# Optimization experiments

Hardware: AMD Instinct MI355X
Metric: run time of the kernel (lower is better)

Reference implementation:

```python
import jax, jax.numpy as jnp
import numpy as np

B = 32768
SEQ_LEN = 24
H = 64            # HIDDEN_DIM
SLOTS = 8         # MEMORY_SLOTS
VOCAB = 64        # VOCAB_SIZE


def setup_inputs() -> dict:
    key = jax.random.key(0)
    ks = jax.random.split(key, 8)
    seqs = jax.random.randint(ks[0], (B, SEQ_LEN), 0, VOCAB, dtype=jnp.int64)
    query_tok = jax.random.randint(ks[1], (B,), 0, VOCAB + 2, dtype=jnp.int64)
    embed = jax.random.normal(ks[2], (VOCAB + 2, H), dtype=jnp.float32) * 0.05
    gw1 = jax.random.normal(ks[3], (2 * H, 32), dtype=jnp.float32) / np.sqrt(2 * H)
    gb1 = jnp.zeros((32,), jnp.float32)
    gw2 = jax.random.normal(ks[4], (32, 1), dtype=jnp.float32) / np.sqrt(32)
    gb2 = jnp.zeros((1,), jnp.float32)
    rw1 = jax.random.normal(ks[5], (2 * H, H), dtype=jnp.float32) / np.sqrt(2 * H)
    rb1 = jnp.zeros((H,), jnp.float32)
    rw2 = jax.random.normal(ks[6], (H, VOCAB), dtype=jnp.float32) / np.sqrt(H)
    rb2 = jnp.zeros((VOCAB,), jnp.float32)
    return {"seqs": seqs, "query_tok": query_tok, "embed": embed,
            "gw1": gw1, "gb1": gb1, "gw2": gw2, "gb2": gb2,
            "rw1": rw1, "rb1": rb1, "rw2": rw2, "rb2": rb2}


def reference(seqs, query_tok, embed, gw1, gb1, gw2, gb2, rw1, rb1, rw2, rb2):
    Bb = seqs.shape[0]
    T = SEQ_LEN - 1  # model writes tokens 0..SEQ_LEN-2 into memory
    embs = embed[seqs[:, :T]]                     # [B, T, H]
    batch_idx = jnp.arange(Bb)

    def step(mem, xs):
        t, emb = xs                               # emb: [B, H]
        ctx = jnp.broadcast_to(emb[:, None, :], mem.shape)
        pair = jnp.concatenate([ctx, mem], axis=-1)        # [B, S, 2H]
        h = jax.nn.relu(pair @ gw1 + gb1)                  # [B, S, 32]
        score = jax.nn.sigmoid(h @ gw2 + gb2)[..., 0]      # [B, S]
        # while memory not full, fill slot t; otherwise evict argmax score
        idx = jnp.where(t < SLOTS, t, jnp.argmax(score, axis=1))
        mem = mem.at[batch_idx, idx].set(emb)
        return mem, None

    mem0 = jnp.zeros((Bb, SLOTS, H), embed.dtype)
    mem, _ = jax.lax.scan(step, mem0, (jnp.arange(T), jnp.swapaxes(embs, 0, 1)))

    summary = mem.mean(axis=1)                    # [B, H]  (memory is full: T > SLOTS)
    q = embed[query_tok]                          # [B, H]
    x = jnp.concatenate([q, summary], axis=-1)    # [B, 2H]
    logits = jax.nn.relu(x @ rw1 + rb1) @ rw2 + rb2   # [B, VOCAB]
    return logits
```

## Files before the change

kernel.cpp:

```cpp
#include <hip/hip_runtime.h>
#include <math.h>

typedef __attribute__((ext_vector_type(8))) _Float16 f16x8;
typedef __attribute__((ext_vector_type(4))) float f32x4;

#define TSTEPS 23

#define WSB_Z  0
#define WSB_B1 16384
#define WSB_W2 37888
#define WSB_U  47104
#define WSB_V  55296

__global__ __launch_bounds__(256) void pre_tables(
    const float* __restrict__ embed, const float* __restrict__ gw1,
    const float* __restrict__ rw1, const float* __restrict__ rb1,
    const float* __restrict__ rw2, char* __restrict__ wsc)
{
    __shared__ float sEmb[66 * 64];
    __shared__ float sW[128 * 64];
    __shared__ float sRb1[64];

    const int tid = threadIdx.x;
    const int blk = blockIdx.x;

    if (blk < 16) {
        {
            const float4* es = (const float4*)embed;
            float4* ed = (float4*)sEmb;
            for (int i = tid; i < 1056; i += 256) ed[i] = es[i];
            const float4* gs = (const float4*)gw1;
            float4* gd = (float4*)sW;
            for (int i = tid; i < 1024; i += 256) gd[i] = gs[i];
        }
        __syncthreads();
        const int e = blk * 256 + tid;
        const int row = (e >> 5) & 63, j = e & 31;
        const int ofs = (e < 2048) ? 0 : 64;
        float acc = 0.f;
        const float* er = sEmb + row * 64;
        #pragma unroll
        for (int k = 0; k < 64; ++k)
            acc = fmaf(er[k], sW[(ofs + k) * 32 + j], acc);
        float* dst = (float*)(wsc + ((e < 2048) ? WSB_U : WSB_V));
        dst[e & 2047] = acc;
    } else if (blk < 49) {
        {
            const float4* es = (const float4*)embed;
            float4* ed = (float4*)sEmb;
            for (int i = tid; i < 1056; i += 256) ed[i] = es[i];
            const float4* rs = (const float4*)rw1;
            float4* rd = (float4*)sW;
            for (int i = tid; i < 2048; i += 256) rd[i] = rs[i];
            if (tid < 64) sRb1[tid] = rb1[tid];
        }
        __syncthreads();
        const int e = (blk - 16) * 256 + tid;
        if (e < 8320) {
            const int n = e & 63, k = e >> 6;
            float acc;
            if (k < 64) {
                acc = 0.f;
                const float* er = sEmb + k * 64;
                #pragma unroll
                for (int m = 0; m < 64; ++m)
                    acc = fmaf(er[m], sW[(64 + m) * 64 + n], acc);
                acc *= 0.125f * 256.f;
            } else {
                const int t = k - 64;
                acc = sRb1[n];
                const float* er = sEmb + t * 64;
                #pragma unroll
                for (int m = 0; m < 64; ++m)
                    acc = fmaf(er[m], sW[m * 64 + n], acc);
                acc *= 256.f;
            }
            ((_Float16*)(wsc + WSB_B1))[n * 168 + k] = (_Float16)acc;
        }
    } else {
        _Float16* w2t = (_Float16*)(wsc + WSB_W2);
        for (int e = tid; e < 4096; e += 256) {
            const int n = e & 63, j = e >> 6;
            w2t[n * 72 + j] = (_Float16)rw2[j * 64 + n];
        }
        _Float16* b1 = (_Float16*)(wsc + WSB_B1);
        for (int e = tid; e < 2432; e += 256) {
            const int n = e / 38, k = 130 + (e - n * 38);
            b1[n * 168 + k] = (_Float16)0.f;
        }
    }
}

__global__ __launch_bounds__(256) void pre_z(
    const float* __restrict__ gb1, const float* __restrict__ gw2,
    const float* __restrict__ gb2, char* __restrict__ wsc)
{
    __shared__ float sU[64 * 33];
    __shared__ float sV[64 * 33];
    __shared__ float sG1[32];
    __shared__ float sG2[32];

    const int tid = threadIdx.x;
    const float* u = (const float*)(wsc + WSB_U);
    const float* v = (const float*)(wsc + WSB_V);
    for (int i = tid; i < 2048; i += 256) {
        sU[(i >> 5) * 33 + (i & 31)] = u[i];
        sV[(i >> 5) * 33 + (i & 31)] = v[i];
    }
    if (tid < 32) { sG1[tid] = gb1[tid]; sG2[tid] = gw2[tid]; }
    __syncthreads();

    const int idx = blockIdx.x * 256 + tid;
    const int c = idx >> 6, s = idx & 63;
    double z = (double)gb2[0];
    #pragma unroll
    for (int j = 0; j < 32; ++j) {
        const double a = (double)sU[c * 33 + j] + (double)sV[s * 33 + j] + (double)sG1[j];
        if (a > 0.0) z += a * (double)sG2[j];
    }
    ((float*)(wsc + WSB_Z))[idx] = (float)(1.0 / (1.0 + exp(-z)));
}

__global__ __launch_bounds__(256, 2) void sm_main(
    const int* __restrict__ seqs, const int* __restrict__ qtok,
    const float* __restrict__ rb2, const char* __restrict__ wsc,
    float* __restrict__ out)
{
    __shared__ __align__(16) float     sZ[64 * 64];
    __shared__ __align__(16) _Float16  sB1[64 * 168];
    __shared__ __align__(16) _Float16  sA[64 * 168];
    __shared__ __align__(16) _Float16  sW2[64 * 72];
    __shared__ __align__(16) _Float16  sH[64 * 72];
    __shared__ unsigned sTokPk[64 * 6];
    __shared__ float sRb2[64];

    const int tid = threadIdx.x;
    const int base = blockIdx.x * 64;

    {
        const float4* zsrc = (const float4*)(wsc + WSB_Z);
        float4* zdst = (float4*)sZ;
        for (int i = tid; i < 1024; i += 256) zdst[i] = zsrc[i];
        const int4* sq = (const int4*)(seqs + base * 24);
        for (int g = tid; g < 384; g += 256) {
            const int4 w = sq[g];
            sTokPk[g] = (unsigned)w.x | ((unsigned)w.y << 8) |
                        ((unsigned)w.z << 16) | ((unsigned)w.w << 24);
        }
        if (tid < 64) sRb2[tid] = rb2[tid];
    }
    int qt = 0;
    if (tid < 64) qt = qtok[base + tid];
    __syncthreads();

    unsigned lo = 0, hi = 0;
    if (tid < 64) {
        const unsigned char* tk = ((const unsigned char*)sTokPk) + tid * 24;
        lo = sTokPk[tid * 6 + 0];
        hi = sTokPk[tid * 6 + 1];
        #pragma unroll
        for (int t = 8; t < TSTEPS; ++t) {
            const int c = tk[t];
            const float* zr = sZ + c * 64;
            float b = zr[lo & 63]; int am = 0; float z;
            z = zr[(lo >> 8) & 63];  if (z > b) { b = z; am = 1; }
            z = zr[(lo >> 16) & 63]; if (z > b) { b = z; am = 2; }
            z = zr[lo >> 24];        if (z > b) { b = z; am = 3; }
            z = zr[hi & 63];         if (z > b) { b = z; am = 4; }
            z = zr[(hi >> 8) & 63];  if (z > b) { b = z; am = 5; }
            z = zr[(hi >> 16) & 63]; if (z > b) { b = z; am = 6; }
            z = zr[hi >> 24];        if (z > b) { b = z; am = 7; }
            const unsigned cb = (unsigned)c;
            if (am < 4) { const int sh = am * 8; lo = (lo & ~(255u << sh)) | (cb << sh); }
            else        { const int sh = am * 8 - 32; hi = (hi & ~(255u << sh)) | (cb << sh); }
        }
    } else {
        const int t2 = tid - 64;
        const float4* b1s = (const float4*)(wsc + WSB_B1);
        float4* b1d = (float4*)sB1;
        for (int i = t2; i < 1344; i += 192) b1d[i] = b1s[i];
        const float4* w2s = (const float4*)(wsc + WSB_W2);
        float4* w2d = (float4*)sW2;
        for (int i = t2; i < 576; i += 192) w2d[i] = w2s[i];
        const float4 z4 = {0.f, 0.f, 0.f, 0.f};
        float4* ad = (float4*)sA;
        for (int i = t2; i < 1344; i += 192) ad[i] = z4;
    }
    __syncthreads();

    if (tid < 64) {
        int t_[8] = { (int)(lo & 63), (int)((lo >> 8) & 63), (int)((lo >> 16) & 63), (int)(lo >> 24),
                      (int)(hi & 63), (int)((hi >> 8) & 63), (int)((hi >> 16) & 63), (int)(hi >> 24) };
        int tot[8] = {1, 1, 1, 1, 1, 1, 1, 1};
        #pragma unroll
        for (int i = 0; i < 8; ++i)
            #pragma unroll
            for (int j = i + 1; j < 8; ++j) {
                const int eq = (t_[i] == t_[j]);
                tot[i] += eq; tot[j] += eq;
            }
        _Float16* arow = sA + tid * 168;
        #pragma unroll
        for (int i = 0; i < 8; ++i) arow[t_[i]] = (_Float16)(float)tot[i];
        arow[64 + qt] = (_Float16)1.0f;
    }
    __syncthreads();

    const int lane = tid & 63;
    const int w = tid >> 6;
    const int c16 = lane & 15, g = lane >> 4;
    const int arow = w * 16 + c16;
    f32x4 a0 = {0.f, 0.f, 0.f, 0.f}, a1 = a0, a2 = a0, a3 = a0;
    #pragma unroll
    for (int ks = 0; ks < 5; ++ks) {
        const int ko = ks * 32 + g * 8;
        const f16x8 af = *(const f16x8*)&sA[arow * 168 + ko];
        const f16x8 b0 = *(const f16x8*)&sB1[(c16) * 168 + ko];
        const f16x8 b1 = *(const f16x8*)&sB1[(16 + c16) * 168 + ko];
        const f16x8 b2 = *(const f16x8*)&sB1[(32 + c16) * 168 + ko];
        const f16x8 b3 = *(const f16x8*)&sB1[(48 + c16) * 168 + ko];
        a0 = __builtin_amdgcn_mfma_f32_16x16x32_f16(af, b0, a0, 0, 0, 0);
        a1 = __builtin_amdgcn_mfma_f32_16x16x32_f16(af, b1, a1, 0, 0, 0);
        a2 = __builtin_amdgcn_mfma_f32_16x16x32_f16(af, b2, a2, 0, 0, 0);
        a3 = __builtin_amdgcn_mfma_f32_16x16x32_f16(af, b3, a3, 0, 0, 0);
    }
    {
        const int rbase = w * 16 + g * 4;
        #pragma unroll
        for (int j = 0; j < 4; ++j) {
            _Float16* hr = sH + (rbase + j) * 72;
            const float v0 = a0[j], v1 = a1[j], v2 = a2[j], v3 = a3[j];
            hr[c16]      = (_Float16)(v0 > 0.f ? v0 : 0.f);
            hr[16 + c16] = (_Float16)(v1 > 0.f ? v1 : 0.f);
            hr[32 + c16] = (_Float16)(v2 > 0.f ? v2 : 0.f);
            hr[48 + c16] = (_Float16)(v3 > 0.f ? v3 : 0.f);
        }
    }
    __syncthreads();

    f32x4 d0 = {0.f, 0.f, 0.f, 0.f}, d1 = d0, d2 = d0, d3 = d0;
    #pragma unroll
    for (int ks = 0; ks < 2; ++ks) {
        const int ko = ks * 32 + g * 8;
        const f16x8 af = *(const f16x8*)&sH[arow * 72 + ko];
        const f16x8 b0 = *(const f16x8*)&sW2[(c16) * 72 + ko];
        const f16x8 b1 = *(const f16x8*)&sW2[(16 + c16) * 72 + ko];
        const f16x8 b2 = *(const f16x8*)&sW2[(32 + c16) * 72 + ko];
        const f16x8 b3 = *(const f16x8*)&sW2[(48 + c16) * 72 + ko];
        d0 = __builtin_amdgcn_mfma_f32_16x16x32_f16(af, b0, d0, 0, 0, 0);
        d1 = __builtin_amdgcn_mfma_f32_16x16x32_f16(af, b1, d1, 0, 0, 0);
        d2 = __builtin_amdgcn_mfma_f32_16x16x32_f16(af, b2, d2, 0, 0, 0);
        d3 = __builtin_amdgcn_mfma_f32_16x16x32_f16(af, b3, d3, 0, 0, 0);
    }
    float* sOut = (float*)(void*)sA;
    {
        const int rbase = w * 16 + g * 4;
        #pragma unroll
        for (int j = 0; j < 4; ++j) {
            float* orow = sOut + (rbase + j) * 68;
            orow[c16]      = d0[j] * (1.f / 256.f) + sRb2[c16];
            orow[16 + c16] = d1[j] * (1.f / 256.f) + sRb2[16 + c16];
            orow[32 + c16] = d2[j] * (1.f / 256.f) + sRb2[32 + c16];
            orow[48 + c16] = d3[j] * (1.f / 256.f) + sRb2[48 + c16];
        }
    }
    __syncthreads();

    #pragma unroll
    for (int r2 = 0; r2 < 4; ++r2) {
        const int idx = r2 * 256 + tid;
        const int row = idx >> 4, c4 = idx & 15;
        *(float4*)(out + (size_t)(base + row) * 64 + c4 * 4) =
            *(const float4*)&sOut[row * 68 + c4 * 4];
    }
}

extern "C" void kernel_launch(void* const* d_in, const int* in_sizes, int n_in,
                              void* d_out, int out_size, void* d_ws, size_t ws_size,
                              hipStream_t stream)
{
    const int* seqs    = (const int*)d_in[0];
    const int* qtok    = (const int*)d_in[1];
    const float* embed = (const float*)d_in[2];
    const float* gw1   = (const float*)d_in[3];
    const float* gb1   = (const float*)d_in[4];
    const float* gw2   = (const float*)d_in[5];
    const float* gb2   = (const float*)d_in[6];
    const float* rw1   = (const float*)d_in[7];
    const float* rb1   = (const float*)d_in[8];
    const float* rw2   = (const float*)d_in[9];
    const float* rb2   = (const float*)d_in[10];
    char* wsc  = (char*)d_ws;
    float* out = (float*)d_out;
    const int B = in_sizes[1];

    pre_tables<<<50, 256, 0, stream>>>(embed, gw1, rw1, rb1, rw2, wsc);
    pre_z<<<16, 256, 0, stream>>>(gb1, gw2, gb2, wsc);
    sm_main<<<B / 64, 256, 0, stream>>>(seqs, qtok, rb2, wsc, out);
}
```

Measured before the change: 23.22 us.

## Fuse gate-score precompute kernels and double rows per main block

Merges the pre_tables and pre_z kernels into one pre_all kernel. Each of its first 16 blocks computes its own U slice, the full V table in shared memory, and the sigmoid score table directly, which removes one launch and the workspace round trip. The main kernel now handles 128 rows per 512-thread block and loads tokens straight into registers instead of staging them in shared memory. The weight table loads now run before the eviction loop and no longer overlap with it. Every block in the fused kernel recomputes V redundantly, and the larger shared footprint may lower occupancy.

```diff
diff --git a/kernel.cpp b/kernel.cpp
--- a/kernel.cpp
+++ b/kernel.cpp
@@ -9,16 +9,19 @@
 #define WSB_Z  0
 #define WSB_B1 16384
 #define WSB_W2 37888
-#define WSB_U  47104
-#define WSB_V  55296
-
-__global__ __launch_bounds__(256) void pre_tables(
+
+__global__ __launch_bounds__(256) void pre_all(
     const float* __restrict__ embed, const float* __restrict__ gw1,
-    const float* __restrict__ rw1, const float* __restrict__ rb1,
-    const float* __restrict__ rw2, char* __restrict__ wsc)
+    const float* __restrict__ gb1, const float* __restrict__ gw2,
+    const float* __restrict__ gb2, const float* __restrict__ rw1,
+    const float* __restrict__ rb1, const float* __restrict__ rw2,
+    char* __restrict__ wsc)
 {
     __shared__ float sEmb[66 * 64];
     __shared__ float sW[128 * 64];
+    __shared__ float sV[64 * 33];
+    __shared__ float sU[4 * 32];
+    __shared__ float sG[65];
     __shared__ float sRb1[64];
 
     const int tid = threadIdx.x;
@@ -28,22 +31,45 @@
         {
             const float4* es = (const float4*)embed;
             float4* ed = (float4*)sEmb;
-            for (int i = tid; i < 1056; i += 256) ed[i] = es[i];
+            for (int i = tid; i < 1024; i += 256) ed[i] = es[i];
             const float4* gs = (const float4*)gw1;
             float4* gd = (float4*)sW;
             for (int i = tid; i < 1024; i += 256) gd[i] = gs[i];
+            if (tid < 32) { sG[tid] = gb1[tid]; sG[32 + tid] = gw2[tid]; }
+            if (tid == 64) sG[64] = gb2[0];
         }
         __syncthreads();
-        const int e = blk * 256 + tid;
-        const int row = (e >> 5) & 63, j = e & 31;
-        const int ofs = (e < 2048) ? 0 : 64;
-        float acc = 0.f;
-        const float* er = sEmb + row * 64;
-        #pragma unroll
-        for (int k = 0; k < 64; ++k)
-            acc = fmaf(er[k], sW[(ofs + k) * 32 + j], acc);
-        float* dst = (float*)(wsc + ((e < 2048) ? WSB_U : WSB_V));
-        dst[e & 2047] = acc;
+        #pragma unroll
+        for (int i = 0; i < 8; ++i) {
+            const int e = tid + i * 256;
+            const int s = e >> 5, j = e & 31;
+            float acc = 0.f;
+            const float* er = sEmb + s * 64;
+            #pragma unroll
+            for (int k = 0; k < 64; ++k)
+                acc = fmaf(er[k], sW[(64 + k) * 32 + j], acc);
+            sV[s * 33 + j] = acc;
+        }
+        if (tid < 128) {
+            const int cc = tid >> 5, j = tid & 31;
+            const int c = blk * 4 + cc;
+            float acc = 0.f;
+            const float* er = sEmb + c * 64;
+            #pragma unroll
+            for (int k = 0; k < 64; ++k)
+                acc = fmaf(er[k], sW[k * 32 + j], acc);
+            sU[cc * 32 + j] = acc;
+        }
+        __syncthreads();
+        const int cc = tid >> 6, s = tid & 63;
+        const int c = blk * 4 + cc;
+        double z = (double)sG[64];
+        #pragma unroll
+        for (int j = 0; j < 32; ++j) {
+            const double a = (double)sU[cc * 32 + j] + (double)sV[s * 33 + j] + (double)sG[j];
+            if (a > 0.0) z += a * (double)sG[32 + j];
+        }
+        ((float*)(wsc + WSB_Z))[c * 64 + s] = (float)(1.0 / (1.0 + exp(-z)));
     } else if (blk < 49) {
         {
             const float4* es = (const float4*)embed;
@@ -91,76 +117,58 @@
     }
 }
 
-__global__ __launch_bounds__(256) void pre_z(
-    const float* __restrict__ gb1, const float* __restrict__ gw2,
-    const float* __restrict__ gb2, char* __restrict__ wsc)
-{
-    __shared__ float sU[64 * 33];
-    __shared__ float sV[64 * 33];
-    __shared__ float sG1[32];
-    __shared__ float sG2[32];
-
-    const int tid = threadIdx.x;
-    const float* u = (const float*)(wsc + WSB_U);
-    const float* v = (const float*)(wsc + WSB_V);
-    for (int i = tid; i < 2048; i += 256) {
-        sU[(i >> 5) * 33 + (i & 31)] = u[i];
-        sV[(i >> 5) * 33 + (i & 31)] = v[i];
-    }
-    if (tid < 32) { sG1[tid] = gb1[tid]; sG2[tid] = gw2[tid]; }
-    __syncthreads();
-
-    const int idx = blockIdx.x * 256 + tid;
-    const int c = idx >> 6, s = idx & 63;
-    double z = (double)gb2[0];
-    #pragma unroll
-    for (int j = 0; j < 32; ++j) {
-        const double a = (double)sU[c * 33 + j] + (double)sV[s * 33 + j] + (double)sG1[j];
-        if (a > 0.0) z += a * (double)sG2[j];
-    }
-    ((float*)(wsc + WSB_Z))[idx] = (float)(1.0 / (1.0 + exp(-z)));
-}
-
-__global__ __launch_bounds__(256, 2) void sm_main(
+#define ROWS 128
+
+__global__ __launch_bounds__(512, 2) void sm_main(
     const int* __restrict__ seqs, const int* __restrict__ qtok,
     const float* __restrict__ rb2, const char* __restrict__ wsc,
     float* __restrict__ out)
 {
     __shared__ __align__(16) float     sZ[64 * 64];
     __shared__ __align__(16) _Float16  sB1[64 * 168];
-    __shared__ __align__(16) _Float16  sA[64 * 168];
+    __shared__ __align__(16) _Float16  sA[128 * 168];
     __shared__ __align__(16) _Float16  sW2[64 * 72];
-    __shared__ __align__(16) _Float16  sH[64 * 72];
-    __shared__ unsigned sTokPk[64 * 6];
+    __shared__ __align__(16) _Float16  sH[128 * 72];
     __shared__ float sRb2[64];
 
     const int tid = threadIdx.x;
-    const int base = blockIdx.x * 64;
+    const int base = blockIdx.x * ROWS;
+
+    unsigned pk[6];
+    int qt = 0;
+    if (tid < ROWS) {
+        const int4* sq = (const int4*)(seqs + (size_t)(base + tid) * 24);
+        #pragma unroll
+        for (int i = 0; i < 6; ++i) {
+            const int4 w4 = sq[i];
+            pk[i] = (unsigned)w4.x | ((unsigned)w4.y << 8) |
+                    ((unsigned)w4.z << 16) | ((unsigned)w4.w << 24);
+        }
+        qt = qtok[base + tid];
+    }
 
     {
         const float4* zsrc = (const float4*)(wsc + WSB_Z);
         float4* zdst = (float4*)sZ;
-        for (int i = tid; i < 1024; i += 256) zdst[i] = zsrc[i];
-        const int4* sq = (const int4*)(seqs + base * 24);
-        for (int g = tid; g < 384; g += 256) {
-            const int4 w = sq[g];
-            sTokPk[g] = (unsigned)w.x | ((unsigned)w.y << 8) |
-                        ((unsigned)w.z << 16) | ((unsigned)w.w << 24);
-        }
+        for (int i = tid; i < 1024; i += 512) zdst[i] = zsrc[i];
+        const float4* b1s = (const float4*)(wsc + WSB_B1);
+        float4* b1d = (float4*)sB1;
+        for (int i = tid; i < 1344; i += 512) b1d[i] = b1s[i];
+        const float4* w2s = (const float4*)(wsc + WSB_W2);
+        float4* w2d = (float4*)sW2;
+        for (int i = tid; i < 576; i += 512) w2d[i] = w2s[i];
+        const float4 z4 = {0.f, 0.f, 0.f, 0.f};
+        float4* ad = (float4*)sA;
+        for (int i = tid; i < 2688; i += 512) ad[i] = z4;
         if (tid < 64) sRb2[tid] = rb2[tid];
     }
-    int qt = 0;
-    if (tid < 64) qt = qtok[base + tid];
-    __syncthreads();
-
-    unsigned lo = 0, hi = 0;
-    if (tid < 64) {
-        const unsigned char* tk = ((const unsigned char*)sTokPk) + tid * 24;
-        lo = sTokPk[tid * 6 + 0];
-        hi = sTokPk[tid * 6 + 1];
+    __syncthreads();
+
+    if (tid < ROWS) {
+        unsigned lo = pk[0], hi = pk[1];
         #pragma unroll
         for (int t = 8; t < TSTEPS; ++t) {
-            const int c = tk[t];
+            const int c = (int)((pk[t >> 2] >> ((t & 3) * 8)) & 255u);
             const float* zr = sZ + c * 64;
             float b = zr[lo & 63]; int am = 0; float z;
             z = zr[(lo >> 8) & 63];  if (z > b) { b = z; am = 1; }
@@ -174,21 +182,6 @@
             if (am < 4) { const int sh = am * 8; lo = (lo & ~(255u << sh)) | (cb << sh); }
             else        { const int sh = am * 8 - 32; hi = (hi & ~(255u << sh)) | (cb << sh); }
         }
-    } else {
-        const int t2 = tid - 64;
-        const float4* b1s = (const float4*)(wsc + WSB_B1);
-        float4* b1d = (float4*)sB1;
-        for (int i = t2; i < 1344; i += 192) b1d[i] = b1s[i];
-        const float4* w2s = (const float4*)(wsc + WSB_W2);
-        float4* w2d = (float4*)sW2;
-        for (int i = t2; i < 576; i += 192) w2d[i] = w2s[i];
-        const float4 z4 = {0.f, 0.f, 0.f, 0.f};
-        float4* ad = (float4*)sA;
-        for (int i = t2; i < 1344; i += 192) ad[i] = z4;
-    }
-    __syncthreads();
-
-    if (tid < 64) {
         int t_[8] = { (int)(lo & 63), (int)((lo >> 8) & 63), (int)((lo >> 16) & 63), (int)(lo >> 24),
                       (int)(hi & 63), (int)((hi >> 8) & 63), (int)((hi >> 16) & 63), (int)(hi >> 24) };
         int tot[8] = {1, 1, 1, 1, 1, 1, 1, 1};
@@ -268,7 +261,7 @@
 
     #pragma unroll
     for (int r2 = 0; r2 < 4; ++r2) {
-        const int idx = r2 * 256 + tid;
+        const int idx = r2 * 512 + tid;
         const int row = idx >> 4, c4 = idx & 15;
         *(float4*)(out + (size_t)(base + row) * 64 + c4 * 4) =
             *(const float4*)&sOut[row * 68 + c4 * 4];
@@ -294,7 +287,6 @@
     float* out = (float*)d_out;
     const int B = in_sizes[1];
 
-    pre_tables<<<50, 256, 0, stream>>>(embed, gw1, rw1, rb1, rw2, wsc);
-    pre_z<<<16, 256, 0, stream>>>(gb1, gw2, gb2, wsc);
-    sm_main<<<B / 64, 256, 0, stream>>>(seqs, qtok, rb2, wsc, out);
+    pre_all<<<50, 256, 0, stream>>>(embed, gw1, gb1, gw2, gb2, rw1, rb1, rw2, wsc);
+    sm_main<<<B / ROWS, 512, 0, stream>>>(seqs, qtok, rb2, wsc, out);
 }
```

Result: no change. 22.82 us (-1.7%).
